# Kernel tuning notes

Hardware: AMD Instinct MI355X
Metric: run time of the kernel (lower is better)

## Reference

```python
import jax, jax.numpy as jnp
import numpy as np

G = 16          # GroupNorm groups
EPS = 1e-5


def setup_inputs() -> dict:
    key = jax.random.key(0)
    ks = jax.random.split(key, 6)
    B, C, H, W = 2, 256, 96, 96
    O = 256
    x = jax.random.normal(ks[0], (B, C, H, W), dtype=jnp.float32)
    offset = jax.random.normal(ks[1], (B, 18, H, W), dtype=jnp.float32)
    mask = jax.random.uniform(ks[2], (B, 9, H, W), dtype=jnp.float32)
    fan_in = C * 9
    weight = jax.random.normal(ks[3], (O, C, 3, 3), dtype=jnp.float32) / np.sqrt(fan_in)
    bias = jnp.zeros((O,), dtype=jnp.float32)
    gamma = jnp.ones((O,), dtype=jnp.float32)
    beta = jnp.zeros((O,), dtype=jnp.float32)
    return {"x": x, "offset": offset, "mask": mask, "weight": weight,
            "bias": bias, "gamma": gamma, "beta": beta}


def _mdcn_gn(x, offset, mask, weight, bias, gamma, beta):
    B, C, H, W = x.shape
    O = weight.shape[0]
    K = 9
    # offsets: mmcv layout [y0,x0,y1,x1,...] per kernel point k = kh*3+kw
    off = offset.reshape(B, K, 2, H, W)
    off_y, off_x = off[:, :, 0], off[:, :, 1]            # [B,K,H,W]
    ky = (jnp.arange(K) // 3 - 1).astype(x.dtype)        # kernel dy, pad=1
    kx = (jnp.arange(K) % 3 - 1).astype(x.dtype)
    hh = jnp.arange(H, dtype=x.dtype)[:, None]
    ww = jnp.arange(W, dtype=x.dtype)[None, :]
    py = hh[None, None] + ky[:, None, None] + off_y      # [B,K,H,W] sample y
    px = ww[None, None] + kx[:, None, None] + off_x      # [B,K,H,W] sample x

    y0 = jnp.floor(py)
    x0 = jnp.floor(px)
    dy = py - y0
    dx = px - x0
    y0i = y0.astype(jnp.int32)
    x0i = x0.astype(jnp.int32)

    xf = x.reshape(B, C, H * W)

    def gather(yi, xi):
        # zero-padded bilinear corner: out-of-range corners contribute 0
        valid = ((yi >= 0) & (yi < H) & (xi >= 0) & (xi < W)).astype(x.dtype)
        yc = jnp.clip(yi, 0, H - 1)
        xc = jnp.clip(xi, 0, W - 1)
        idx = (yc * W + xc).reshape(B, 1, K * H * W)
        v = jnp.take_along_axis(xf, idx, axis=2).reshape(B, C, K, H, W)
        return v * valid.reshape(B, 1, K, H, W)

    w00 = ((1 - dy) * (1 - dx))[:, None]                 # [B,1,K,H,W]
    w01 = ((1 - dy) * dx)[:, None]
    w10 = (dy * (1 - dx))[:, None]
    w11 = (dy * dx)[:, None]
    val = (gather(y0i, x0i) * w00 + gather(y0i, x0i + 1) * w01 +
           gather(y0i + 1, x0i) * w10 + gather(y0i + 1, x0i + 1) * w11)
    val = val * mask[:, None]                            # modulation [B,C,K,H,W]

    out = jnp.einsum('ock,bckhw->bohw', weight.reshape(O, C, K), val)
    out = out + bias[None, :, None, None]

    # GroupNorm(16, O)
    xg = out.reshape(B, G, O // G, H, W)
    mean = xg.mean(axis=(2, 3, 4), keepdims=True)
    var = jnp.mean((xg - mean) ** 2, axis=(2, 3, 4), keepdims=True)
    xn = ((xg - mean) * jax.lax.rsqrt(var + EPS)).reshape(B, O, H, W)
    return xn * gamma[None, :, None, None] + beta[None, :, None, None]


def reference(x, offset, mask, weight, bias, gamma, beta):
    return _mdcn_gn(x, offset, mask, weight, bias, gamma, beta)
```

## Files before the change

kernel.cpp:

```cpp
#include <hip/hip_runtime.h>
#include <hip/hip_fp16.h>

typedef _Float16 f16;
typedef __attribute__((ext_vector_type(2))) _Float16 h2v;
typedef __attribute__((ext_vector_type(8))) _Float16 f16x8;
typedef __attribute__((ext_vector_type(4))) float f32x4;

#define HW_    9216
#define PADP   8
#define XP_    112
#define XPXP_  12544
#define NSTEP  36
#define NMT    288
#define XT_BYTES   12845056
#define BMAT_BYTES 1179648
#define ATILE_B    294912

#define GLOAD_LDS16(g, l) \
  __builtin_amdgcn_global_load_lds((const __attribute__((address_space(1))) void*)(g), \
                                   (__attribute__((address_space(3))) void*)(l), 16, 0, 0)

union U4 { uint4 u; h2v h[4]; f16x8 v; };
union U1 { unsigned u; h2v h; };

__global__ __launch_bounds__(256) void k_prep_x(const float* __restrict__ x, f16* __restrict__ xT) {
    __shared__ float tile[64 * 97];
    int blk = blockIdx.x;
    int cg  = blk & 3;
    int y   = (blk >> 2) % 96;
    int b   = blk / 384;
    int t   = threadIdx.x;
    const float* src = x + (((size_t)(b*256 + cg*64))*96 + y)*96;
    for (int e = t; e < 6144; e += 256) {
        int c = e / 96, wcol = e - c*96;
        tile[c*97 + wcol] = src[(size_t)c*HW_ + wcol];
    }
    __syncthreads();
    f16* dst = xT + ((size_t)b*XPXP_ + (size_t)(y+PADP)*XP_ + PADP)*256 + cg*64;
    for (int e = t; e < 6144; e += 256) {
        int wcol = e >> 6, c = e & 63;
        dst[(size_t)wcol*256 + c] = (f16)tile[c*97 + wcol];
    }
}

__global__ __launch_bounds__(256) void k_prep_w(const float* __restrict__ wgt, f16* __restrict__ bmat) {
    int id = blockIdx.x*256 + threadIdx.x;
    int s = id >> 14, r = id & 16383;
    int o = r >> 6,  j = r & 63;
    int c = ((s & 3) << 6) + j;
    int k = s >> 2;
    float v = wgt[((size_t)o*256 + c)*9 + k];
    int oh = o >> 7, op = o & 127;
    int swz = ((op << 6) + j) ^ ((op & 7) << 3);
    bmat[(s << 14) + (oh << 13) + swz] = (f16)v;
}

__global__ __launch_bounds__(256, 6) void k_sample(
        const f16* __restrict__ xT, const float* __restrict__ offs,
        const float* __restrict__ maskp, f16* __restrict__ Ag, int mt0, int nblk)
{
    __shared__ int   geo_i[64];
    __shared__ uint4 geo_w[64];

    int blk0 = blockIdx.x;
    int blk  = (blk0 & 7)*(nblk >> 3) + (blk0 >> 3);
    int mtl  = blk / 9;
    int k    = blk - mtl*9;
    int mt   = mt0 + mtl;
    int b    = mt / 144;

    int tid = threadIdx.x;
    if (tid < 64) {
        int hw = mt*64 + tid - b*HW_;
        int h = hw / 96, w = hw - h*96;
        float offy = offs[((size_t)b*18 + 2*k    )*HW_ + hw];
        float offx = offs[((size_t)b*18 + 2*k + 1)*HW_ + hw];
        float mv   = maskp[((size_t)b*9 + k)*HW_ + hw];
        int ky = k/3 - 1, kx = k - (k/3)*3 - 1;
        float py = (float)(h + ky) + offy;
        float px = (float)(w + kx) + offx;
        py = fminf(fmaxf(py, -7.5f), 102.4f);
        px = fminf(fmaxf(px, -7.5f), 102.4f);
        float y0 = floorf(py), x0 = floorf(px);
        float dy = py - y0,   dx = px - x0;
        geo_i[tid] = (((int)y0 + PADP)*XP_ + ((int)x0 + PADP)) << 9;
        float w00v = (1.f-dy)*(1.f-dx)*mv, w01v = (1.f-dy)*dx*mv;
        float w10v = dy*(1.f-dx)*mv,       w11v = dy*dx*mv;
        U1 p0, p1, p2, p3;
        p0.h = h2v{(f16)w00v, (f16)w00v};
        p1.h = h2v{(f16)w01v, (f16)w01v};
        p2.h = h2v{(f16)w10v, (f16)w10v};
        p3.h = h2v{(f16)w11v, (f16)w11v};
        geo_w[tid] = uint4{p0.u, p1.u, p2.u, p3.u};
    }
    __syncthreads();

    const char* xbC = (const char*)xT + (size_t)b*XPXP_*512;
    char* dst = (char*)Ag + (size_t)mtl*ATILE_B;

    #pragma unroll
    for (int j = 0; j < 8; ++j) {
        int item = tid + j*256;
        int row = item >> 5, chunk = item & 31;
        const char* p = xbC + geo_i[row] + (chunk << 4);
        U4 t0, t1, t2, t3, oo;
        t0.u = *(const uint4*)(p);
        t1.u = *(const uint4*)(p + 512);
        t2.u = *(const uint4*)(p + XP_*512);
        t3.u = *(const uint4*)(p + XP_*512 + 512);
        U4 w4; w4.u = geo_w[row];
        h2v w00 = w4.h[0], w01 = w4.h[1], w10 = w4.h[2], w11 = w4.h[3];
        #pragma unroll
        for (int q = 0; q < 4; ++q)
            oo.h[q] = w00*t0.h[q] + w01*t1.h[q] + w10*t2.h[q] + w11*t3.h[q];
        int s = k*4 + (chunk >> 3);
        int byteA = ((row << 7) + ((chunk & 7) << 4)) ^ ((row & 7) << 4);
        *(uint4*)(dst + (size_t)s*8192 + byteA) = oo.u;
    }
}

__global__ __launch_bounds__(256, 3) void k_gemm(
        const f16* __restrict__ Ag, const f16* __restrict__ bmat,
        const float* __restrict__ bias, float* __restrict__ out,
        float* __restrict__ part, int mt0, int nblk)
{
    __shared__ __align__(16) char LDS[2][24576];
    __shared__ float psum[2][8][2];

    int blk0 = blockIdx.x;
    int blk  = (blk0 & 7)*(nblk >> 3) + (blk0 >> 3);
    int mtl  = blk >> 1;
    int oh   = blk & 1;
    int mt   = mt0 + mtl;

    int tid = threadIdx.x, lane = tid & 63, wid = tid >> 6;
    int wm = wid >> 1, wn = wid & 1;

    const char* aG = (const char*)Ag + (size_t)mtl*ATILE_B;
    const char* bG = (const char*)bmat + (oh << 14);
    char* ldsB = &LDS[0][0];

    f32x4 acc[2][4];
    #pragma unroll
    for (int i = 0; i < 2; ++i)
        #pragma unroll
        for (int j = 0; j < 4; ++j) acc[i][j] = (f32x4){0.f,0.f,0.f,0.f};

#define GSTAGE(s_, buf_) do { \
    const char* ga_ = aG + (size_t)(s_)*8192; \
    GLOAD_LDS16(ga_ + (tid << 4),           ldsB + (buf_)*24576 + (tid << 4)); \
    GLOAD_LDS16(ga_ + ((tid + 256) << 4),   ldsB + (buf_)*24576 + ((tid + 256) << 4)); \
    const char* gb_ = bG + (size_t)(s_)*32768; \
    _Pragma("unroll") \
    for (int i_ = 0; i_ < 4; ++i_) \
      GLOAD_LDS16(gb_ + ((tid + i_*256) << 4), ldsB + (buf_)*24576 + 8192 + ((tid + i_*256) << 4)); \
  } while (0)

    GSTAGE(0, 0);
    for (int s = 0; s < NSTEP; ++s) {
        int cur = s & 1;
        __syncthreads();
        if (s + 1 < NSTEP) GSTAGE(s + 1, cur ^ 1);
        const char* Lc = ldsB + cur*24576;
        #pragma unroll
        for (int kh = 0; kh < 2; ++kh) {
            int kb = (kh << 6) + ((lane >> 4) << 4);
            int r0 = wm*32 + (lane & 15);
            int r1 = r0 + 16;
            f16x8 a0 = *(const f16x8*)(Lc + (((r0 << 7) + kb) ^ ((r0 & 7) << 4)));
            f16x8 a1 = *(const f16x8*)(Lc + (((r1 << 7) + kb) ^ ((r1 & 7) << 4)));
            #pragma unroll
            for (int fn = 0; fn < 4; ++fn) {
                int op = wn*64 + fn*16 + (lane & 15);
                f16x8 bf = *(const f16x8*)(Lc + 8192 + (((op << 7) + kb) ^ ((op & 7) << 4)));
                acc[0][fn] = __builtin_amdgcn_mfma_f32_16x16x32_f16(a0, bf, acc[0][fn], 0, 0, 0);
                acc[1][fn] = __builtin_amdgcn_mfma_f32_16x16x32_f16(a1, bf, acc[1][fn], 0, 0, 0);
            }
        }
    }

    int ol = lane & 15;
    int qr = (lane >> 4) << 2;
    int b  = mt / 144;
    int hwb = mt*64 - b*HW_;
    #pragma unroll
    for (int fm = 0; fm < 2; ++fm) {
        int mrow = wm*32 + fm*16 + qr;
        #pragma unroll
        for (int fn = 0; fn < 4; ++fn) {
            int o = oh*128 + wn*64 + fn*16 + ol;
            float bv = bias[o];
            f32x4 a = acc[fm][fn];
            a[0] += bv; a[1] += bv; a[2] += bv; a[3] += bv;
            acc[fm][fn] = a;
            *(float4*)(out + ((size_t)(b*256 + o))*HW_ + hwb + mrow)
                = make_float4(a[0], a[1], a[2], a[3]);
        }
    }
    #pragma unroll
    for (int fn = 0; fn < 4; ++fn) {
        float s1 = 0.f, s2 = 0.f;
        #pragma unroll
        for (int fm = 0; fm < 2; ++fm) {
            f32x4 a = acc[fm][fn];
            s1 += a[0]+a[1]+a[2]+a[3];
            s2 += a[0]*a[0]+a[1]*a[1]+a[2]*a[2]+a[3]*a[3];
        }
        #pragma unroll
        for (int m = 32; m > 0; m >>= 1) {
            s1 += __shfl_xor(s1, m);
            s2 += __shfl_xor(s2, m);
        }
        if (lane == 0) { psum[wm][wn*4+fn][0] = s1; psum[wm][wn*4+fn][1] = s2; }
    }
    __syncthreads();
    if (tid < 8) {
        float s1 = psum[0][tid][0] + psum[1][tid][0];
        float s2 = psum[0][tid][1] + psum[1][tid][1];
        part[(size_t)(mt*2 + oh)*16 + tid*2]     = s1;
        part[(size_t)(mt*2 + oh)*16 + tid*2 + 1] = s2;
    }
#undef GSTAGE
}

__global__ __launch_bounds__(256) void k_finalize(const float* __restrict__ part, float* __restrict__ stats) {
    int bg = blockIdx.x, b = bg >> 4, g = bg & 15;
    int oh = g >> 3, gl = g & 7;
    float s1 = 0.f, s2 = 0.f;
    if (threadIdx.x < 144) {
        int mt = b*144 + threadIdx.x;
        const float* p = part + (size_t)(mt*2 + oh)*16 + gl*2;
        s1 = p[0]; s2 = p[1];
    }
    __shared__ float a1[256], a2[256];
    a1[threadIdx.x] = s1; a2[threadIdx.x] = s2;
    __syncthreads();
    for (int off = 128; off > 0; off >>= 1) {
        if (threadIdx.x < off) { a1[threadIdx.x] += a1[threadIdx.x+off]; a2[threadIdx.x] += a2[threadIdx.x+off]; }
        __syncthreads();
    }
    if (threadIdx.x == 0) {
        float inv_n = 1.f/147456.f;
        float mean = a1[0]*inv_n;
        float var  = fmaxf(a2[0]*inv_n - mean*mean, 0.f);
        stats[bg*2]   = mean;
        stats[bg*2+1] = rsqrtf(var + 1e-5f);
    }
}

__global__ __launch_bounds__(256) void k_norm(float* __restrict__ out, const float* __restrict__ stats,
                                              const float* __restrict__ gamma, const float* __restrict__ beta) {
    int i4 = blockIdx.x*256 + threadIdx.x;
    int p  = i4 / 2304;
    int o  = p & 255;
    float mean = stats[(p>>4)*2], rstd = stats[(p>>4)*2 + 1];
    float ga = gamma[o], be = beta[o];
    float4 v = ((const float4*)out)[i4];
    v.x = (v.x-mean)*rstd*ga + be;
    v.y = (v.y-mean)*rstd*ga + be;
    v.z = (v.z-mean)*rstd*ga + be;
    v.w = (v.w-mean)*rstd*ga + be;
    ((float4*)out)[i4] = v;
}

extern "C" void kernel_launch(void* const* d_in, const int* in_sizes, int n_in,
                              void* d_out, int out_size, void* d_ws, size_t ws_size,
                              hipStream_t stream) {
    const float* x      = (const float*)d_in[0];
    const float* offset = (const float*)d_in[1];
    const float* mask   = (const float*)d_in[2];
    const float* weight = (const float*)d_in[3];
    const float* bias   = (const float*)d_in[4];
    const float* gamma  = (const float*)d_in[5];
    const float* beta   = (const float*)d_in[6];
    float* out = (float*)d_out;

    char* ws = (char*)d_ws;
    f16*   xT    = (f16*)ws;
    f16*   bmat  = (f16*)(ws + XT_BYTES);
    float* part  = (float*)(ws + XT_BYTES + BMAT_BYTES);
    float* stats = (float*)(ws + XT_BYTES + BMAT_BYTES + 36864);
    char*  Ag    = ws + 14061824;

    size_t needA = (size_t)NMT * ATILE_B;
    size_t avail = ws_size > 14061824 ? ws_size - 14061824 : 0;
    int P = (avail >= needA) ? 1 : ((avail >= needA/2) ? 2 : 4);

    (void)hipMemsetAsync(xT, 0, XT_BYTES, stream);
    k_prep_x<<<768, 256, 0, stream>>>(x, xT);
    k_prep_w<<<2304, 256, 0, stream>>>(weight, bmat);
    int mtn = NMT / P;
    for (int p = 0; p < P; ++p) {
        k_sample<<<mtn*9, 256, 0, stream>>>(xT, offset, mask, (f16*)Ag, p*mtn, mtn*9);
        k_gemm<<<mtn*2, 256, 0, stream>>>((f16*)Ag, bmat, bias, out, part, p*mtn, mtn*2);
    }
    k_finalize<<<32, 256, 0, stream>>>(part, stats);
    k_norm<<<4608, 256, 0, stream>>>(out, stats, gamma, beta);
}
```

Measured before the change: 84.93 us.

## Triple-buffer GEMM with MFMA-fragment layouts and fp16 intermediate output

The A and B operands are stored in a pre-arranged MFMA fragment layout, so LDS reads become contiguous per-lane loads with no swizzle arithmetic. The GEMM main loop now uses smaller K-steps with three LDS buffers, prefetching two stages ahead with explicit vmcnt waits, raw barriers and setprio, and it allows higher occupancy. The pre-norm conv output is written as fp16 to a workspace buffer and read back by the norm kernel, which halves that intermediate traffic. This costs precision in the stored pre-norm values and more workspace, and the k_prep_w weight-repack kernel is rewritten to match the new B layout.

```diff
diff --git a/kernel.cpp b/kernel.cpp
--- a/kernel.cpp
+++ b/kernel.cpp
@@ -10,18 +10,20 @@
 #define PADP   8
 #define XP_    112
 #define XPXP_  12544
-#define NSTEP  36
+#define NSTEP  72
 #define NMT    288
 #define XT_BYTES   12845056
 #define BMAT_BYTES 1179648
 #define ATILE_B    294912
+#define OUTH_BYTES 9437184
 
 #define GLOAD_LDS16(g, l) \
   __builtin_amdgcn_global_load_lds((const __attribute__((address_space(1))) void*)(g), \
                                    (__attribute__((address_space(3))) void*)(l), 16, 0, 0)
 
-union U4 { uint4 u; h2v h[4]; f16x8 v; };
+union U4 { uint4 u; h2v h[4]; f16x8 v; f16 f[8]; };
 union U1 { unsigned u; h2v h; };
+union UO { ushort4 s; f16 f[4]; };
 
 __global__ __launch_bounds__(256) void k_prep_x(const float* __restrict__ x, f16* __restrict__ xT) {
     __shared__ float tile[64 * 97];
@@ -45,14 +47,14 @@
 
 __global__ __launch_bounds__(256) void k_prep_w(const float* __restrict__ wgt, f16* __restrict__ bmat) {
     int id = blockIdx.x*256 + threadIdx.x;
-    int s = id >> 14, r = id & 16383;
-    int o = r >> 6,  j = r & 63;
-    int c = ((s & 3) << 6) + j;
-    int k = s >> 2;
-    float v = wgt[((size_t)o*256 + c)*9 + k];
-    int oh = o >> 7, op = o & 127;
-    int swz = ((op << 6) + j) ^ ((op & 7) << 3);
-    bmat[(s << 14) + (oh << 13) + swz] = (f16)v;
+    int o = id / 2304;
+    int rem = id - o*2304;
+    int c = rem / 9;
+    int k = rem - c*9;
+    int s  = k*8 + (c >> 5);
+    int oh = o >> 7, fn = (o >> 4) & 7, r = o & 15;
+    int cp = c & 31, q = cp >> 3, e = cp & 7;
+    bmat[(size_t)(s*2 + oh)*4096 + fn*512 + (q*16 + r)*8 + e] = (f16)wgt[id];
 }
 
 __global__ __launch_bounds__(256, 6) void k_sample(
@@ -113,18 +115,18 @@
         #pragma unroll
         for (int q = 0; q < 4; ++q)
             oo.h[q] = w00*t0.h[q] + w01*t1.h[q] + w10*t2.h[q] + w11*t3.h[q];
-        int s = k*4 + (chunk >> 3);
-        int byteA = ((row << 7) + ((chunk & 7) << 4)) ^ ((row & 7) << 4);
-        *(uint4*)(dst + (size_t)s*8192 + byteA) = oo.u;
-    }
-}
-
-__global__ __launch_bounds__(256, 3) void k_gemm(
+        int s = k*8 + (chunk >> 2);
+        int off = ((row >> 4) << 10) + (((row & 15) + ((chunk & 3) << 4)) << 4);
+        *(uint4*)(dst + (size_t)s*4096 + off) = oo.u;
+    }
+}
+
+__global__ __launch_bounds__(256, 4) void k_gemm(
         const f16* __restrict__ Ag, const f16* __restrict__ bmat,
-        const float* __restrict__ bias, float* __restrict__ out,
+        const float* __restrict__ bias, f16* __restrict__ outh,
         float* __restrict__ part, int mt0, int nblk)
 {
-    __shared__ __align__(16) char LDS[2][24576];
+    __shared__ __align__(16) char LDS[3*12288];
     __shared__ float psum[2][8][2];
 
     int blk0 = blockIdx.x;
@@ -137,8 +139,8 @@
     int wm = wid >> 1, wn = wid & 1;
 
     const char* aG = (const char*)Ag + (size_t)mtl*ATILE_B;
-    const char* bG = (const char*)bmat + (oh << 14);
-    char* ldsB = &LDS[0][0];
+    const char* bG = (const char*)bmat + (oh << 13);
+    char* ldsC = &LDS[0];
 
     f32x4 acc[2][4];
     #pragma unroll
@@ -146,38 +148,50 @@
         #pragma unroll
         for (int j = 0; j < 4; ++j) acc[i][j] = (f32x4){0.f,0.f,0.f,0.f};
 
-#define GSTAGE(s_, buf_) do { \
-    const char* ga_ = aG + (size_t)(s_)*8192; \
-    GLOAD_LDS16(ga_ + (tid << 4),           ldsB + (buf_)*24576 + (tid << 4)); \
-    GLOAD_LDS16(ga_ + ((tid + 256) << 4),   ldsB + (buf_)*24576 + ((tid + 256) << 4)); \
-    const char* gb_ = bG + (size_t)(s_)*32768; \
+#define STAGE(t_, BUF) do { \
+    const char* ga_ = aG + ((size_t)(t_) << 12); \
+    GLOAD_LDS16(ga_ + (tid << 4),            ldsC + (BUF)*12288 + (tid << 4)); \
+    const char* gb_ = bG + ((size_t)(t_) << 14); \
+    GLOAD_LDS16(gb_ + (tid << 4),            ldsC + (BUF)*12288 + 4096 + (tid << 4)); \
+    GLOAD_LDS16(gb_ + 4096 + (tid << 4),     ldsC + (BUF)*12288 + 8192 + (tid << 4)); \
+  } while (0)
+
+#define MM(CUR) do { \
+    const char* Lc_ = ldsC + (CUR)*12288; \
+    f16x8 a0_ = *(const f16x8*)(Lc_ + ((wm*2 + 0) << 10) + (lane << 4)); \
+    f16x8 a1_ = *(const f16x8*)(Lc_ + ((wm*2 + 1) << 10) + (lane << 4)); \
     _Pragma("unroll") \
-    for (int i_ = 0; i_ < 4; ++i_) \
-      GLOAD_LDS16(gb_ + ((tid + i_*256) << 4), ldsB + (buf_)*24576 + 8192 + ((tid + i_*256) << 4)); \
+    for (int j_ = 0; j_ < 4; ++j_) { \
+      f16x8 bf_ = *(const f16x8*)(Lc_ + 4096 + ((wn*4 + j_) << 10) + (lane << 4)); \
+      acc[0][j_] = __builtin_amdgcn_mfma_f32_16x16x32_f16(a0_, bf_, acc[0][j_], 0, 0, 0); \
+      acc[1][j_] = __builtin_amdgcn_mfma_f32_16x16x32_f16(a1_, bf_, acc[1][j_], 0, 0, 0); \
+    } \
   } while (0)
 
-    GSTAGE(0, 0);
-    for (int s = 0; s < NSTEP; ++s) {
-        int cur = s & 1;
-        __syncthreads();
-        if (s + 1 < NSTEP) GSTAGE(s + 1, cur ^ 1);
-        const char* Lc = ldsB + cur*24576;
-        #pragma unroll
-        for (int kh = 0; kh < 2; ++kh) {
-            int kb = (kh << 6) + ((lane >> 4) << 4);
-            int r0 = wm*32 + (lane & 15);
-            int r1 = r0 + 16;
-            f16x8 a0 = *(const f16x8*)(Lc + (((r0 << 7) + kb) ^ ((r0 & 7) << 4)));
-            f16x8 a1 = *(const f16x8*)(Lc + (((r1 << 7) + kb) ^ ((r1 & 7) << 4)));
-            #pragma unroll
-            for (int fn = 0; fn < 4; ++fn) {
-                int op = wn*64 + fn*16 + (lane & 15);
-                f16x8 bf = *(const f16x8*)(Lc + 8192 + (((op << 7) + kb) ^ ((op & 7) << 4)));
-                acc[0][fn] = __builtin_amdgcn_mfma_f32_16x16x32_f16(a0, bf, acc[0][fn], 0, 0, 0);
-                acc[1][fn] = __builtin_amdgcn_mfma_f32_16x16x32_f16(a1, bf, acc[1][fn], 0, 0, 0);
-            }
-        }
-    }
+#define ITER(s_, CUR, NBUF, PF, VN) do { \
+    asm volatile("s_waitcnt vmcnt(" VN ")" ::: "memory"); \
+    __builtin_amdgcn_s_barrier(); \
+    __builtin_amdgcn_sched_barrier(0); \
+    if (PF) STAGE((s_)+2, NBUF); \
+    __builtin_amdgcn_s_setprio(1); \
+    MM(CUR); \
+    __builtin_amdgcn_s_setprio(0); \
+  } while (0)
+
+    STAGE(0, 0);
+    STAGE(1, 1);
+    for (int sb = 0; sb < 69; sb += 3) {
+        ITER(sb,   0, 2, 1, "3");
+        ITER(sb+1, 1, 0, 1, "3");
+        ITER(sb+2, 2, 1, 1, "3");
+    }
+    ITER(69, 0, 2, 1, "3");
+    ITER(70, 1, 0, 0, "3");
+    ITER(71, 2, 1, 0, "0");
+
+#undef STAGE
+#undef MM
+#undef ITER
 
     int ol = lane & 15;
     int qr = (lane >> 4) << 2;
@@ -187,22 +201,24 @@
     for (int fm = 0; fm < 2; ++fm) {
         int mrow = wm*32 + fm*16 + qr;
         #pragma unroll
-        for (int fn = 0; fn < 4; ++fn) {
-            int o = oh*128 + wn*64 + fn*16 + ol;
+        for (int j = 0; j < 4; ++j) {
+            int o = oh*128 + wn*64 + j*16 + ol;
             float bv = bias[o];
-            f32x4 a = acc[fm][fn];
+            f32x4 a = acc[fm][j];
             a[0] += bv; a[1] += bv; a[2] += bv; a[3] += bv;
-            acc[fm][fn] = a;
-            *(float4*)(out + ((size_t)(b*256 + o))*HW_ + hwb + mrow)
-                = make_float4(a[0], a[1], a[2], a[3]);
+            acc[fm][j] = a;
+            UO ov;
+            ov.f[0] = (f16)a[0]; ov.f[1] = (f16)a[1];
+            ov.f[2] = (f16)a[2]; ov.f[3] = (f16)a[3];
+            *(ushort4*)(outh + ((size_t)(b*256 + o))*HW_ + hwb + mrow) = ov.s;
         }
     }
     #pragma unroll
-    for (int fn = 0; fn < 4; ++fn) {
+    for (int j = 0; j < 4; ++j) {
         float s1 = 0.f, s2 = 0.f;
         #pragma unroll
         for (int fm = 0; fm < 2; ++fm) {
-            f32x4 a = acc[fm][fn];
+            f32x4 a = acc[fm][j];
             s1 += a[0]+a[1]+a[2]+a[3];
             s2 += a[0]*a[0]+a[1]*a[1]+a[2]*a[2]+a[3]*a[3];
         }
@@ -211,7 +227,7 @@
             s1 += __shfl_xor(s1, m);
             s2 += __shfl_xor(s2, m);
         }
-        if (lane == 0) { psum[wm][wn*4+fn][0] = s1; psum[wm][wn*4+fn][1] = s2; }
+        if (lane == 0) { psum[wm][wn*4+j][0] = s1; psum[wm][wn*4+j][1] = s2; }
     }
     __syncthreads();
     if (tid < 8) {
@@ -220,7 +236,6 @@
         part[(size_t)(mt*2 + oh)*16 + tid*2]     = s1;
         part[(size_t)(mt*2 + oh)*16 + tid*2 + 1] = s2;
     }
-#undef GSTAGE
 }
 
 __global__ __launch_bounds__(256) void k_finalize(const float* __restrict__ part, float* __restrict__ stats) {
@@ -248,19 +263,22 @@
     }
 }
 
-__global__ __launch_bounds__(256) void k_norm(float* __restrict__ out, const float* __restrict__ stats,
+__global__ __launch_bounds__(256) void k_norm(const f16* __restrict__ outh, float* __restrict__ out,
+                                              const float* __restrict__ stats,
                                               const float* __restrict__ gamma, const float* __restrict__ beta) {
-    int i4 = blockIdx.x*256 + threadIdx.x;
-    int p  = i4 / 2304;
+    int i8 = blockIdx.x*256 + threadIdx.x;
+    int p  = i8 / 1152;
     int o  = p & 255;
     float mean = stats[(p>>4)*2], rstd = stats[(p>>4)*2 + 1];
-    float ga = gamma[o], be = beta[o];
-    float4 v = ((const float4*)out)[i4];
-    v.x = (v.x-mean)*rstd*ga + be;
-    v.y = (v.y-mean)*rstd*ga + be;
-    v.z = (v.z-mean)*rstd*ga + be;
-    v.w = (v.w-mean)*rstd*ga + be;
-    ((float4*)out)[i4] = v;
+    float ga = gamma[o]*rstd, be = beta[o] - mean*rstd*gamma[o];
+    U4 v; v.u = ((const uint4*)outh)[i8];
+    float4 o0, o1;
+    o0.x = (float)v.f[0]*ga + be; o0.y = (float)v.f[1]*ga + be;
+    o0.z = (float)v.f[2]*ga + be; o0.w = (float)v.f[3]*ga + be;
+    o1.x = (float)v.f[4]*ga + be; o1.y = (float)v.f[5]*ga + be;
+    o1.z = (float)v.f[6]*ga + be; o1.w = (float)v.f[7]*ga + be;
+    ((float4*)out)[i8*2]     = o0;
+    ((float4*)out)[i8*2 + 1] = o1;
 }
 
 extern "C" void kernel_launch(void* const* d_in, const int* in_sizes, int n_in,
@@ -280,10 +298,12 @@
     f16*   bmat  = (f16*)(ws + XT_BYTES);
     float* part  = (float*)(ws + XT_BYTES + BMAT_BYTES);
     float* stats = (float*)(ws + XT_BYTES + BMAT_BYTES + 36864);
-    char*  Ag    = ws + 14061824;
+    f16*   outh  = (f16*)(ws + 14061824);
+    char*  Ag    = ws + 14061824 + OUTH_BYTES;
 
     size_t needA = (size_t)NMT * ATILE_B;
-    size_t avail = ws_size > 14061824 ? ws_size - 14061824 : 0;
+    size_t base  = 14061824 + (size_t)OUTH_BYTES;
+    size_t avail = ws_size > base ? ws_size - base : 0;
     int P = (avail >= needA) ? 1 : ((avail >= needA/2) ? 2 : 4);
 
     (void)hipMemsetAsync(xT, 0, XT_BYTES, stream);
@@ -292,8 +312,8 @@
     int mtn = NMT / P;
     for (int p = 0; p < P; ++p) {
         k_sample<<<mtn*9, 256, 0, stream>>>(xT, offset, mask, (f16*)Ag, p*mtn, mtn*9);
-        k_gemm<<<mtn*2, 256, 0, stream>>>((f16*)Ag, bmat, bias, out, part, p*mtn, mtn*2);
+        k_gemm<<<mtn*2, 256, 0, stream>>>((f16*)Ag, bmat, bias, outh, part, p*mtn, mtn*2);
     }
     k_finalize<<<32, 256, 0, stream>>>(part, stats);
-    k_norm<<<4608, 256, 0, stream>>>(out, stats, gamma, beta);
-}
+    k_norm<<<2304, 256, 0, stream>>>(outh, out, stats, gamma, beta);
+}
```

New measurement: 94.71 us. 11.5% more time.
